# Performance work log

Hardware: AMD Instinct MI355X
Metric: run time of the kernel (lower is better)

Reference implementation:

```python
import jax, jax.numpy as jnp
import numpy as np

B, N, K, IN = 8, 2048, 8, 5
BN = B * N

def _lin(k, i, o):
    s = 1.0 / np.sqrt(i)
    return jax.random.uniform(k, (i, o), jnp.float32, -s, s)

def setup_inputs() -> dict:
    key = jax.random.key(0)
    ks = jax.random.split(key, 12)
    inp = {"points": jax.random.normal(ks[0], (B, N, IN), jnp.float32)}
    dims = [(IN * 2, 64), (64 * 2, 128), (128 * 2, 256)]
    for n, (i, o) in enumerate(dims, 1):
        inp[f"W{n}"] = _lin(ks[n], i, o)
        inp[f"b{n}"] = jnp.zeros((o,), jnp.float32)
        inp[f"g{n}"] = jnp.ones((o,), jnp.float32)
        inp[f"be{n}"] = jnp.zeros((o,), jnp.float32)
    inp["Wf1"] = _lin(ks[10], 448, 512); inp["bf1"] = jnp.zeros((512,), jnp.float32)
    inp["gf"] = jnp.ones((512,), jnp.float32); inp["bef"] = jnp.zeros((512,), jnp.float32)
    inp["Wf2"] = _lin(ks[11], 512, 128); inp["bf2"] = jnp.zeros((128,), jnp.float32)
    return inp

def _lrelu(x):
    return jnp.where(x >= 0, x, 0.2 * x)

def _bn(x, g, b, eps=1e-5):
    # BatchNorm1d in training mode: per-feature batch statistics
    m = x.mean(0)
    v = x.var(0)
    return (x - m) * jax.lax.rsqrt(v + eps) * g + b

def _knn_idx(pos):
    # pos: [B,N,3] -> neighbor indices [B,N,K], self excluded
    sq = (pos * pos).sum(-1)
    d = sq[:, :, None] + sq[:, None, :] - 2.0 * jnp.einsum('bnc,bmc->bnm', pos, pos)
    d = d + jnp.eye(N, dtype=d.dtype) * 1e10  # exclude self
    _, idx = jax.lax.top_k(-d, K)
    return idx

def _edge_conv(x, src, dst, W, b, g, be):
    # PyG EdgeConv: msg = nn(cat[x_i, x_j - x_i]); aggr='max' at target i
    xc = x[dst]
    xn = x[src]
    h = jnp.concatenate([xc, xn - xc], axis=-1) @ W + b
    h = _bn(_lrelu(h), g, be)
    return jax.ops.segment_max(h, dst, num_segments=BN)

def reference(points, W1, b1, g1, be1, W2, b2, g2, be2, W3, b3, g3, be3,
              Wf1, bf1, gf, bef, Wf2, bf2):
    pos = points[..., :3]                      # [B,N,3]
    idx = _knn_idx(pos)                        # [B,N,K]
    offs = (jnp.arange(B) * N)[:, None, None]
    src = (idx + offs).reshape(-1)             # neighbor (source) node ids [E]
    dst = jnp.repeat(jnp.arange(BN), K)        # center (target) node ids [E]
    x = points.reshape(BN, IN)
    x1 = _edge_conv(x, src, dst, W1, b1, g1, be1)   # [BN,64]
    x2 = _edge_conv(x1, src, dst, W2, b2, g2, be2)  # [BN,128]
    x3 = _edge_conv(x2, src, dst, W3, b3, g3, be3)  # [BN,256]
    xs = jnp.concatenate([x1, x2, x3], axis=-1).reshape(B, N, 448)
    gfeat = xs.max(axis=1)                     # global max pool per cloud [B,448]
    h = _bn(_lrelu(gfeat @ Wf1 + bf1), gf, bef)
    return h @ Wf2 + bf2                       # [B,128]
```

## Files before the change

kernel.cpp:

```cpp
#include <hip/hip_runtime.h>
#include <math.h>

#define B_ 8
#define N_ 2048
#define K_ 8
#define IN_ 5
#define BN_ (B_*N_)
#define NEDGE_ (BN_*K_)
#define GRP 8
#define SEG_ 32
#define CSEG_ (N_/SEG_)
#define CHUNKS_ (N_/GRP)

typedef unsigned short ushort8_ __attribute__((ext_vector_type(8)));
typedef short bf16x8_ __attribute__((ext_vector_type(8)));
typedef float f32x4_ __attribute__((ext_vector_type(4)));

__device__ inline unsigned short f2bf(float f) {
    unsigned int u = __float_as_uint(f);
    u += 0x7fffu + ((u >> 16) & 1u);
    return (unsigned short)(u >> 16);
}
__device__ inline float bf2f(unsigned short h) {
    return __uint_as_float(((unsigned int)h) << 16);
}

__device__ inline unsigned int ord_f32(float f) {
    unsigned int u = __float_as_uint(f);
    return u ^ (((unsigned int)((int)u >> 31)) | 0x80000000u);
}

__global__ __launch_bounds__(256) void knn_part(const float4* __restrict__ P4,
                                                unsigned long long* __restrict__ part) {
    int tid = threadIdx.x;
    int bblk = blockIdx.x >> 3;
    int q = blockIdx.x * 256 + tid;
    int nloc = q & (N_-1);
    int seg = blockIdx.y;

    float4 qp = P4[q];
    float qx2 = -2.0f*qp.x, qy2 = -2.0f*qp.y, qz2 = -2.0f*qp.z;
    float qsq = qp.w;

    unsigned int bd[K_], bi[K_];
#pragma unroll
    for (int k = 0; k < K_; ++k) { bd[k] = 0xFFFFFFFFu; bi[k] = 0xFFFFFFFFu; }

    const float4* __restrict__ cb = P4 + ((size_t)bblk << 11) + (size_t)seg*CSEG_;
    int jbase = seg * CSEG_;

#pragma unroll 8
    for (int jj = 0; jj < CSEG_; ++jj) {
        float4 c = cb[jj];
        float d = qsq + c.w;
        d = fmaf(qx2, c.x, d);
        d = fmaf(qy2, c.y, d);
        d = fmaf(qz2, c.z, d);
        int jg = jbase + jj;
        d = (jg == nloc) ? INFINITY : d;
        unsigned int cd = ord_f32(d);
        unsigned int ci = (unsigned int)jg;
#pragma unroll
        for (int p = 0; p < K_; ++p) {
            bool lt = cd < bd[p];
            unsigned int nd = lt ? cd : bd[p];
            unsigned int xd = lt ? bd[p] : cd;
            unsigned int ni = lt ? ci : bi[p];
            unsigned int xi = lt ? bi[p] : ci;
            bd[p] = nd; cd = xd; bi[p] = ni; ci = xi;
        }
    }
    unsigned long long* op = part + ((size_t)seg * BN_ + q) * K_;
#pragma unroll
    for (int k = 0; k < K_; ++k)
        op[k] = ((unsigned long long)bd[k] << 32) | bi[k];
}

__global__ __launch_bounds__(128) void knn_merge(const unsigned long long* __restrict__ part,
                                                 int* __restrict__ src) {
    int q = blockIdx.x * 128 + threadIdx.x;
    int b = q / N_;
    unsigned long long best[K_];
#pragma unroll
    for (int k = 0; k < K_; ++k) best[k] = ~0ull;
    for (int s = 0; s < SEG_; ++s) {
        const unsigned long long* lp = part + ((size_t)s * BN_ + q) * K_;
#pragma unroll
        for (int k = 0; k < K_; ++k) {
            unsigned long long key = lp[k];
            if (key >= best[K_-1]) break;
            unsigned long long cur = key;
#pragma unroll
            for (int p = 0; p < K_; ++p) {
                unsigned long long lo = best[p] < cur ? best[p] : cur;
                unsigned long long hi = best[p] < cur ? cur : best[p];
                best[p] = lo; cur = hi;
            }
        }
    }
#pragma unroll
    for (int k = 0; k < K_; ++k)
        src[(size_t)q*K_ + k] = b*N_ + (int)(best[k] & 0xFFFFFFFFu);
}

__global__ __launch_bounds__(256) void cast_prep1(const float* __restrict__ X,
                                                  unsigned short* __restrict__ Xh,
                                                  unsigned short* __restrict__ Xl,
                                                  float4* __restrict__ P4,
                                                  const float* __restrict__ W1,
                                                  const float* __restrict__ b1,
                                                  unsigned short* __restrict__ WTh,
                                                  unsigned short* __restrict__ WTl,
                                                  float* __restrict__ cvec) {
    const int total8 = BN_ * 32 / 8;
    int t = blockIdx.x * 256 + threadIdx.x;
    if (t < total8) {
        int m = t >> 2;
        int k0 = (t & 3) * 8;
        ushort8_ vh, vl;
#pragma unroll
        for (int j = 0; j < 8; ++j) {
            int k = k0 + j;
            float v = (k < IN_) ? X[(size_t)m*IN_ + k] : 0.0f;
            unsigned short h = f2bf(v);
            vh[j] = h;
            vl[j] = f2bf(v - bf2f(h));
        }
        *(ushort8_*)(Xh + (size_t)m*32 + k0) = vh;
        *(ushort8_*)(Xl + (size_t)m*32 + k0) = vl;
        if (t < BN_) {
            const float* p = X + (size_t)t*IN_;
            float x = p[0], y = p[1], z = p[2];
            P4[t] = make_float4(x, y, z, x*x + y*y + z*z);
        }
    } else {
        int idx = t - total8;
        const int nWT = 2*64*32;
        if (idx < nWT) {
            int n = idx >> 5;
            int k = idx & 31;
            float val = 0.0f;
            if (k < IN_) {
                if (n < 64) val = W1[(size_t)k*64 + n] - W1[(size_t)(IN_+k)*64 + n];
                else        val = W1[(size_t)(IN_+k)*64 + (n - 64)];
            }
            unsigned short h = f2bf(val);
            WTh[(size_t)n*32 + k] = h;
            WTl[(size_t)n*32 + k] = f2bf(val - bf2f(h));
        } else if (idx < nWT + 64) {
            int c = idx - nWT;
            cvec[c] = b1[c];
        }
    }
}

__global__ __launch_bounds__(256) void prep_layer(const float* __restrict__ W,
                                                  const float* __restrict__ scale,
                                                  const float* __restrict__ shift,
                                                  const float* __restrict__ bias,
                                                  unsigned short* __restrict__ WTh,
                                                  unsigned short* __restrict__ WTl,
                                                  float* __restrict__ cvec,
                                                  int Cin, int C, int Kpad) {
    int idx = blockIdx.x * 256 + threadIdx.x;
    int nWT = 2*C*Kpad;
    if (idx < nWT) {
        int n = idx / Kpad;
        int k = idx % Kpad;
        float val = 0.0f;
        if (k < Cin) {
            float s = scale[k];
            if (n < C) val = s * (W[(size_t)k*C + n] - W[(size_t)(Cin+k)*C + n]);
            else       val = s * W[(size_t)(Cin+k)*C + (n - C)];
        }
        unsigned short h = f2bf(val);
        WTh[(size_t)n*Kpad + k] = h;
        WTl[(size_t)n*Kpad + k] = f2bf(val - bf2f(h));
    } else if (idx < nWT + C) {
        int c = idx - nWT;
        float acc = bias[c];
        for (int d = 0; d < Cin; ++d) acc += shift[d] * W[(size_t)d*C + c];
        cvec[c] = acc;
    }
}

__global__ __launch_bounds__(256) void mfma_dual(const unsigned short* __restrict__ Xh,
                                                 const unsigned short* __restrict__ Xl,
                                                 const unsigned short* __restrict__ WTh,
                                                 const unsigned short* __restrict__ WTl,
                                                 float* __restrict__ PQ, int K, int Ntot,
                                                 int gx) {
    __shared__ unsigned short sXh[128*32], sXl[128*32], sWh[128*32], sWl[128*32];
    int n = blockIdx.x;
    int by = (n & 7) + 8*(n/(8*gx));
    int bx = (n >> 3) % gx;
    int tid = threadIdx.x, l = tid & 63, w = tid >> 6;
    int wr = w >> 1, wc = w & 1;
    int bm = by * 128, bn0 = bx * 128;

    f32x4_ acc[4][4];
#pragma unroll
    for (int i = 0; i < 4; ++i)
#pragma unroll
        for (int j = 0; j < 4; ++j) acc[i][j] = (f32x4_){0.f, 0.f, 0.f, 0.f};

    for (int k0 = 0; k0 < K; k0 += 32) {
#pragma unroll
        for (int i = 0; i < 2; ++i) {
            int idx = tid + i*256;
            int row = idx >> 2;
            int col0 = (idx & 3) * 8;
            size_t gxo = (size_t)(bm  + row)*K + k0 + col0;
            size_t gwo = (size_t)(bn0 + row)*K + k0 + col0;
            int lo_ = ((row << 6) | (col0 << 1)) ^ ((row & 7) << 4);
            *(ushort8_*)((char*)sXh + lo_) = *(const ushort8_*)(Xh + gxo);
            *(ushort8_*)((char*)sXl + lo_) = *(const ushort8_*)(Xl + gxo);
            *(ushort8_*)((char*)sWh + lo_) = *(const ushort8_*)(WTh + gwo);
            *(ushort8_*)((char*)sWl + lo_) = *(const ushort8_*)(WTl + gwo);
        }
        __syncthreads();

        int kb = (l >> 4) << 4;
        bf16x8_ bh[4], bl4[4];
#pragma unroll
        for (int nf = 0; nf < 4; ++nf) {
            int rn = wc*64 + nf*16 + (l & 15);
            int o = ((rn << 6) | kb) ^ ((rn & 7) << 4);
            bh[nf]  = *(const bf16x8_*)((const char*)sWh + o);
            bl4[nf] = *(const bf16x8_*)((const char*)sWl + o);
        }
#pragma unroll
        for (int mf = 0; mf < 4; ++mf) {
            int rm = wr*64 + mf*16 + (l & 15);
            int o = ((rm << 6) | kb) ^ ((rm & 7) << 4);
            bf16x8_ ah = *(const bf16x8_*)((const char*)sXh + o);
            bf16x8_ al = *(const bf16x8_*)((const char*)sXl + o);
#pragma unroll
            for (int nf = 0; nf < 4; ++nf) {
                acc[mf][nf] = __builtin_amdgcn_mfma_f32_16x16x32_bf16(ah, bh[nf],  acc[mf][nf], 0, 0, 0);
                acc[mf][nf] = __builtin_amdgcn_mfma_f32_16x16x32_bf16(ah, bl4[nf], acc[mf][nf], 0, 0, 0);
                acc[mf][nf] = __builtin_amdgcn_mfma_f32_16x16x32_bf16(al, bh[nf],  acc[mf][nf], 0, 0, 0);
            }
        }
        __syncthreads();
    }

    int r0 = (l >> 4) << 2, cB = l & 15;
#pragma unroll
    for (int mf = 0; mf < 4; ++mf)
#pragma unroll
        for (int nf = 0; nf < 4; ++nf) {
            int col = bn0 + wc*64 + nf*16 + cB;
#pragma unroll
            for (int reg = 0; reg < 4; ++reg) {
                int row = bm + wr*64 + mf*16 + r0 + reg;
                PQ[(size_t)row*Ntot + col] = acc[mf][nf][reg];
            }
        }
}

__global__ void combine_kernel(const float* __restrict__ P, const float* __restrict__ Q,
                               const float* __restrict__ cvec, const int* __restrict__ src,
                               unsigned short* __restrict__ Xh_out, unsigned short* __restrict__ Xl_out,
                               float* __restrict__ partial, float* __restrict__ gpart,
                               int C, int S) {
    int pb = blockIdx.x;
    int lb = (pb & 7) * CHUNKS_ + (pb >> 3);
    int c = threadIdx.x;
    int i0 = lb * GRP;
    float cv = cvec[c];
    float sum = 0.f, ssq = 0.f;
    float bmx = -INFINITY;
    for (int g = 0; g < GRP; ++g) {
        int i = i0 + g;
        float p = P[(size_t)i*S + c] + cv;
        float mx = -INFINITY;
#pragma unroll
        for (int k = 0; k < K_; ++k) {
            int s = src[(size_t)i*K_ + k];
            float h = p + Q[(size_t)s*S + c];
            float l = (h >= 0.f) ? h : 0.2f*h;
            sum += l; ssq += l*l;
            mx = fmaxf(mx, l);
        }
        if (Xh_out) {
            unsigned short hh = f2bf(mx);
            Xh_out[(size_t)i*C + c] = hh;
            Xl_out[(size_t)i*C + c] = f2bf(mx - bf2f(hh));
        }
        bmx = fmaxf(bmx, mx);
    }
    gpart[(size_t)lb*C + c] = bmx;
    partial[(size_t)lb*2*C + c]     = sum;
    partial[(size_t)lb*2*C + C + c] = ssq;
}

__global__ __launch_bounds__(256) void reduce_kernel(const float* __restrict__ partial, int nblocks, int C,
                              const float* __restrict__ g, const float* __restrict__ be,
                              float* __restrict__ scale, float* __restrict__ shift) {
    int c = blockIdx.x;
    float s0 = 0.f, s1 = 0.f;
    for (int blk = threadIdx.x; blk < nblocks; blk += 256) {
        s0 += partial[(size_t)blk*2*C + c];
        s1 += partial[(size_t)blk*2*C + C + c];
    }
    __shared__ float l0[256], l1[256];
    l0[threadIdx.x] = s0; l1[threadIdx.x] = s1;
    __syncthreads();
    for (int off = 128; off > 0; off >>= 1) {
        if (threadIdx.x < off) {
            l0[threadIdx.x] += l0[threadIdx.x + off];
            l1[threadIdx.x] += l1[threadIdx.x + off];
        }
        __syncthreads();
    }
    if (threadIdx.x == 0) {
        float mean = l0[0] / (float)NEDGE_;
        float var  = l1[0] / (float)NEDGE_ - mean*mean;
        float sc = g[c] * rsqrtf(var + 1e-5f);
        scale[c] = sc;
        shift[c] = be[c] - mean*sc;
    }
}

__global__ __launch_bounds__(1024) void gmax_finalize(
        const float* __restrict__ gp1, const float* __restrict__ gp2, const float* __restrict__ gp3,
        const float* __restrict__ sc1, const float* __restrict__ sh1,
        const float* __restrict__ sc2, const float* __restrict__ sh2,
        const float* __restrict__ sc3, const float* __restrict__ sh3,
        float* __restrict__ gfeat) {
    int b = blockIdx.x, grp = blockIdx.y;
    const float *gp, *sc, *sh; int C, c0, coff;
    if (grp == 0)      { gp = gp1; sc = sc1; sh = sh1; C = 64;  c0 = 0;            coff = 0;   }
    else if (grp <= 2) { gp = gp2; sc = sc2; sh = sh2; C = 128; c0 = (grp-1)*64;   coff = 64;  }
    else               { gp = gp3; sc = sc3; sh = sh3; C = 256; c0 = (grp-3)*64;   coff = 192; }
    int cl = threadIdx.x & 63;
    int stripe = threadIdx.x >> 6;
    int c = c0 + cl;
    float mx = -INFINITY;
    for (int ch = stripe; ch < CHUNKS_; ch += 16)
        mx = fmaxf(mx, gp[((size_t)b*CHUNKS_ + ch)*C + c]);
    __shared__ float red[16][64];
    red[stripe][cl] = mx;
    __syncthreads();
    for (int off = 8; off > 0; off >>= 1) {
        if (stripe < off) red[stripe][cl] = fmaxf(red[stripe][cl], red[stripe+off][cl]);
        __syncthreads();
    }
    if (stripe == 0)
        gfeat[b*448 + coff + c] = sc[c]*red[0][cl] + sh[c];
}

__global__ __launch_bounds__(256) void final1(const float* __restrict__ gfeat,
                                              const float* __restrict__ Wf1, const float* __restrict__ bf1,
                                              const float* __restrict__ gf, const float* __restrict__ bef,
                                              float* __restrict__ H) {
    __shared__ float gfs[B_][448];
    __shared__ float red[4][64][B_];
    int t = threadIdx.x;
    int cl = t & 63;
    int stripe = t >> 6;
    int c = blockIdx.x * 64 + cl;
    for (int e = t; e < B_*448; e += 256) gfs[e/448][e%448] = gfeat[e];
    __syncthreads();
    float acc[B_] = {};
    for (int d = stripe*112; d < stripe*112 + 112; ++d) {
        float w = Wf1[(size_t)d*512 + c];
#pragma unroll
        for (int r = 0; r < B_; ++r) acc[r] += gfs[r][d] * w;
    }
#pragma unroll
    for (int r = 0; r < B_; ++r) red[stripe][cl][r] = acc[r];
    __syncthreads();
    if (stripe == 0) {
        float v[B_];
        float b1v = bf1[c];
#pragma unroll
        for (int r = 0; r < B_; ++r) {
            float a = red[0][cl][r] + red[1][cl][r] + red[2][cl][r] + red[3][cl][r] + b1v;
            v[r] = (a >= 0.f) ? a : 0.2f*a;
        }
        float mean = 0.f;
#pragma unroll
        for (int r = 0; r < B_; ++r) mean += v[r];
        mean *= (1.0f/B_);
        float var = 0.f;
#pragma unroll
        for (int r = 0; r < B_; ++r) { float dd = v[r] - mean; var += dd*dd; }
        var *= (1.0f/B_);
        float sc = gf[c] * rsqrtf(var + 1e-5f);
        float sh = bef[c] - mean*sc;
#pragma unroll
        for (int r = 0; r < B_; ++r) H[(size_t)r*512 + c] = v[r]*sc + sh;
    }
}

__global__ __launch_bounds__(128) void final2(const float* __restrict__ H,
                                              const float* __restrict__ Wf2, const float* __restrict__ bf2,
                                              float* __restrict__ out) {
    int b = blockIdx.x, c = threadIdx.x;
    __shared__ float hs[512];
    for (int e = c; e < 512; e += 128) hs[e] = H[(size_t)b*512 + e];
    __syncthreads();
    float a = bf2[c];
    for (int d = 0; d < 512; ++d) a += hs[d] * Wf2[(size_t)d*128 + c];
    out[b*128 + c] = a;
}

extern "C" void kernel_launch(void* const* d_in, const int* in_sizes, int n_in,
                              void* d_out, int out_size, void* d_ws, size_t ws_size,
                              hipStream_t stream) {
    (void)in_sizes; (void)n_in; (void)out_size; (void)ws_size;
    const float* points = (const float*)d_in[0];
    const float* W1 = (const float*)d_in[1];  const float* b1 = (const float*)d_in[2];
    const float* g1 = (const float*)d_in[3];  const float* be1 = (const float*)d_in[4];
    const float* W2 = (const float*)d_in[5];  const float* b2 = (const float*)d_in[6];
    const float* g2 = (const float*)d_in[7];  const float* be2 = (const float*)d_in[8];
    const float* W3 = (const float*)d_in[9];  const float* b3 = (const float*)d_in[10];
    const float* g3 = (const float*)d_in[11]; const float* be3 = (const float*)d_in[12];
    const float* Wf1 = (const float*)d_in[13]; const float* bf1 = (const float*)d_in[14];
    const float* gf = (const float*)d_in[15];  const float* bef = (const float*)d_in[16];
    const float* Wf2 = (const float*)d_in[17]; const float* bf2 = (const float*)d_in[18];
    float* out = (float*)d_out;

    size_t off = 0;
    char* base = (char*)d_ws;
    auto carve = [&](size_t bytes) -> void* {
        void* p = base + off;
        off += (bytes + 255) & ~(size_t)255;
        return p;
    };
    int*   src     = (int*)  carve((size_t)NEDGE_ * 4);
    float* PQ      = (float*)carve((size_t)BN_ * 512 * 4);
    float* gp1     = (float*)carve((size_t)(BN_/GRP) * 64 * 4);
    float* gp2     = (float*)carve((size_t)(BN_/GRP) * 128 * 4);
    float* gp3     = (float*)carve((size_t)(BN_/GRP) * 256 * 4);
    unsigned short* XhA = (unsigned short*)carve((size_t)BN_ * 128 * 2);
    unsigned short* XlA = (unsigned short*)carve((size_t)BN_ * 128 * 2);
    unsigned short* XhB = (unsigned short*)carve((size_t)BN_ * 128 * 2);
    unsigned short* XlB = (unsigned short*)carve((size_t)BN_ * 128 * 2);
    unsigned short* WTh = (unsigned short*)carve((size_t)512 * 128 * 2);
    unsigned short* WTl = (unsigned short*)carve((size_t)512 * 128 * 2);
    float4* P4     = (float4*)carve((size_t)BN_ * 16);
    float* cvec    = (float*)carve(256 * 4);
    float* sc1     = (float*)carve(64 * 4);
    float* sh1     = (float*)carve(64 * 4);
    float* sc2     = (float*)carve(128 * 4);
    float* sh2     = (float*)carve(128 * 4);
    float* sc3     = (float*)carve(256 * 4);
    float* sh3     = (float*)carve(256 * 4);
    float* partial = (float*)carve((size_t)(BN_/GRP) * 2 * 256 * 4);
    float* gfeat   = (float*)carve((size_t)B_ * 448 * 4);
    float* H       = (float*)carve((size_t)B_ * 512 * 4);

    cast_prep1<<<(65536 + 4096 + 64 + 255)/256, 256, 0, stream>>>(
        points, XhA, XlA, P4, W1, b1, WTh, WTl, cvec);

    unsigned long long* part = (unsigned long long*)PQ;
    knn_part<<<dim3(BN_/256, SEG_), 256, 0, stream>>>(P4, part);
    knn_merge<<<BN_/128, 128, 0, stream>>>(part, src);

    mfma_dual<<<1*(BN_/128), 256, 0, stream>>>(XhA, XlA, WTh, WTl, PQ, 32, 128, 1);
    combine_kernel<<<BN_/GRP, 64, 0, stream>>>(PQ, PQ + 64, cvec, src, XhB, XlB, partial, gp1, 64, 128);
    reduce_kernel<<<64, 256, 0, stream>>>(partial, BN_/GRP, 64, g1, be1, sc1, sh1);

    prep_layer<<<(2*128*64 + 128 + 255)/256, 256, 0, stream>>>(W2, sc1, sh1, b2, WTh, WTl, cvec, 64, 128, 64);
    mfma_dual<<<2*(BN_/128), 256, 0, stream>>>(XhB, XlB, WTh, WTl, PQ, 64, 256, 2);
    combine_kernel<<<BN_/GRP, 128, 0, stream>>>(PQ, PQ + 128, cvec, src, XhA, XlA, partial, gp2, 128, 256);
    reduce_kernel<<<128, 256, 0, stream>>>(partial, BN_/GRP, 128, g2, be2, sc2, sh2);

    prep_layer<<<(2*256*128 + 256 + 255)/256, 256, 0, stream>>>(W3, sc2, sh2, b3, WTh, WTl, cvec, 128, 256, 128);
    mfma_dual<<<4*(BN_/128), 256, 0, stream>>>(XhA, XlA, WTh, WTl, PQ, 128, 512, 4);
    combine_kernel<<<BN_/GRP, 256, 0, stream>>>(PQ, PQ + 256, cvec, src, nullptr, nullptr, partial, gp3, 256, 512);
    reduce_kernel<<<256, 256, 0, stream>>>(partial, BN_/GRP, 256, g3, be3, sc3, sh3);

    gmax_finalize<<<dim3(B_, 7), 1024, 0, stream>>>(gp1, gp2, gp3,
                                                    sc1, sh1, sc2, sh2, sc3, sh3, gfeat);

    final1<<<8, 256, 0, stream>>>(gfeat, Wf1, bf1, gf, bef, H);
    final2<<<8, 128, 0, stream>>>(H, Wf2, bf2, out);
}
```

Measured before the change: 220.4 us.

## Fuse BN stats reduction with weight prep and widen combine blocks

The per-channel BN reduction and the next layer's weight folding are merged into one bnprep kernel, cutting two launches. The bias/shift constant vector is now computed inside combine_kernel, so the separate cvec pass goes away. combine_kernel always runs 256 threads and splits the points of a group across sub-groups, then does an in-block shared-memory reduction. This raises occupancy for the narrow layers, but every block now redundantly recomputes the cvec dot product. The kNN distance key also drops the order-preserving float transform and compares raw bits, which assumes distances are non-negative.

```diff
diff --git a/kernel.cpp b/kernel.cpp
--- a/kernel.cpp
+++ b/kernel.cpp
@@ -25,11 +25,6 @@
     return __uint_as_float(((unsigned int)h) << 16);
 }
 
-__device__ inline unsigned int ord_f32(float f) {
-    unsigned int u = __float_as_uint(f);
-    return u ^ (((unsigned int)((int)u >> 31)) | 0x80000000u);
-}
-
 __global__ __launch_bounds__(256) void knn_part(const float4* __restrict__ P4,
                                                 unsigned long long* __restrict__ part) {
     int tid = threadIdx.x;
@@ -56,9 +51,9 @@
         d = fmaf(qx2, c.x, d);
         d = fmaf(qy2, c.y, d);
         d = fmaf(qz2, c.z, d);
+        unsigned int cd = __float_as_uint(d);
         int jg = jbase + jj;
-        d = (jg == nloc) ? INFINITY : d;
-        unsigned int cd = ord_f32(d);
+        cd = (jg == nloc) ? 0xFFFFFFFFu : cd;
         unsigned int ci = (unsigned int)jg;
 #pragma unroll
         for (int p = 0; p < K_; ++p) {
@@ -108,10 +103,8 @@
                                                   unsigned short* __restrict__ Xl,
                                                   float4* __restrict__ P4,
                                                   const float* __restrict__ W1,
-                                                  const float* __restrict__ b1,
                                                   unsigned short* __restrict__ WTh,
-                                                  unsigned short* __restrict__ WTl,
-                                                  float* __restrict__ cvec) {
+                                                  unsigned short* __restrict__ WTl) {
     const int total8 = BN_ * 32 / 8;
     int t = blockIdx.x * 256 + threadIdx.x;
     if (t < total8) {
@@ -147,40 +140,76 @@
             unsigned short h = f2bf(val);
             WTh[(size_t)n*32 + k] = h;
             WTl[(size_t)n*32 + k] = f2bf(val - bf2f(h));
-        } else if (idx < nWT + 64) {
-            int c = idx - nWT;
-            cvec[c] = b1[c];
-        }
-    }
-}
-
-__global__ __launch_bounds__(256) void prep_layer(const float* __restrict__ W,
-                                                  const float* __restrict__ scale,
-                                                  const float* __restrict__ shift,
-                                                  const float* __restrict__ bias,
-                                                  unsigned short* __restrict__ WTh,
-                                                  unsigned short* __restrict__ WTl,
-                                                  float* __restrict__ cvec,
-                                                  int Cin, int C, int Kpad) {
-    int idx = blockIdx.x * 256 + threadIdx.x;
-    int nWT = 2*C*Kpad;
-    if (idx < nWT) {
-        int n = idx / Kpad;
-        int k = idx % Kpad;
-        float val = 0.0f;
-        if (k < Cin) {
-            float s = scale[k];
-            if (n < C) val = s * (W[(size_t)k*C + n] - W[(size_t)(Cin+k)*C + n]);
-            else       val = s * W[(size_t)(Cin+k)*C + (n - C)];
-        }
+        }
+    }
+}
+
+__global__ __launch_bounds__(256) void bnprep(const float* __restrict__ partial, int nblocks, int Cprev,
+                                              const float* __restrict__ g, const float* __restrict__ be,
+                                              float* __restrict__ scale, float* __restrict__ shift,
+                                              const float* __restrict__ W, int C, int Kpad,
+                                              unsigned short* __restrict__ WTh,
+                                              unsigned short* __restrict__ WTl) {
+    int k = blockIdx.x;
+    int t = threadIdx.x;
+    float s0 = 0.f, s1 = 0.f;
+    for (int blk = t; blk < nblocks; blk += 256) {
+        s0 += partial[(size_t)blk*2*Cprev + k];
+        s1 += partial[(size_t)blk*2*Cprev + Cprev + k];
+    }
+    __shared__ float l0[256], l1[256];
+    __shared__ float sc_s;
+    l0[t] = s0; l1[t] = s1;
+    __syncthreads();
+    for (int off = 128; off > 0; off >>= 1) {
+        if (t < off) { l0[t] += l0[t + off]; l1[t] += l1[t + off]; }
+        __syncthreads();
+    }
+    if (t == 0) {
+        float mean = l0[0] / (float)NEDGE_;
+        float var  = l1[0] / (float)NEDGE_ - mean*mean;
+        float sc = g[k] * rsqrtf(var + 1e-5f);
+        scale[k] = sc;
+        shift[k] = be[k] - mean*sc;
+        sc_s = sc;
+    }
+    __syncthreads();
+    float s = sc_s;
+    for (int n = t; n < 2*C; n += 256) {
+        float val;
+        if (n < C) val = s * (W[(size_t)k*C + n] - W[(size_t)(Cprev+k)*C + n]);
+        else       val = s * W[(size_t)(Cprev+k)*C + (n - C)];
         unsigned short h = f2bf(val);
         WTh[(size_t)n*Kpad + k] = h;
         WTl[(size_t)n*Kpad + k] = f2bf(val - bf2f(h));
-    } else if (idx < nWT + C) {
-        int c = idx - nWT;
-        float acc = bias[c];
-        for (int d = 0; d < Cin; ++d) acc += shift[d] * W[(size_t)d*C + c];
-        cvec[c] = acc;
+    }
+}
+
+__global__ __launch_bounds__(256) void reduce_kernel(const float* __restrict__ partial, int nblocks, int C,
+                              const float* __restrict__ g, const float* __restrict__ be,
+                              float* __restrict__ scale, float* __restrict__ shift) {
+    int c = blockIdx.x;
+    float s0 = 0.f, s1 = 0.f;
+    for (int blk = threadIdx.x; blk < nblocks; blk += 256) {
+        s0 += partial[(size_t)blk*2*C + c];
+        s1 += partial[(size_t)blk*2*C + C + c];
+    }
+    __shared__ float l0[256], l1[256];
+    l0[threadIdx.x] = s0; l1[threadIdx.x] = s1;
+    __syncthreads();
+    for (int off = 128; off > 0; off >>= 1) {
+        if (threadIdx.x < off) {
+            l0[threadIdx.x] += l0[threadIdx.x + off];
+            l1[threadIdx.x] += l1[threadIdx.x + off];
+        }
+        __syncthreads();
+    }
+    if (threadIdx.x == 0) {
+        float mean = l0[0] / (float)NEDGE_;
+        float var  = l1[0] / (float)NEDGE_ - mean*mean;
+        float sc = g[c] * rsqrtf(var + 1e-5f);
+        scale[c] = sc;
+        shift[c] = be[c] - mean*sc;
     }
 }
 
@@ -259,20 +288,29 @@
         }
 }
 
-__global__ void combine_kernel(const float* __restrict__ P, const float* __restrict__ Q,
-                               const float* __restrict__ cvec, const int* __restrict__ src,
-                               unsigned short* __restrict__ Xh_out, unsigned short* __restrict__ Xl_out,
-                               float* __restrict__ partial, float* __restrict__ gpart,
-                               int C, int S) {
+__global__ __launch_bounds__(256) void combine_kernel(
+        const float* __restrict__ P, const float* __restrict__ Q,
+        const int* __restrict__ src,
+        unsigned short* __restrict__ Xh_out, unsigned short* __restrict__ Xl_out,
+        float* __restrict__ partial, float* __restrict__ gpart,
+        const float* __restrict__ W, const float* __restrict__ bias,
+        const float* __restrict__ shift, int Cin,
+        int C, int S) {
     int pb = blockIdx.x;
     int lb = (pb & 7) * CHUNKS_ + (pb >> 3);
-    int c = threadIdx.x;
-    int i0 = lb * GRP;
-    float cv = cvec[c];
+    int tid = threadIdx.x;
+    int c = tid & (C - 1);
+    int g = tid / C;
+    int PPG = GRP / (256 / C);
+    float cv = bias[c];
+    if (shift)
+        for (int d = 0; d < Cin; ++d) cv += shift[d] * W[(size_t)d*C + c];
+
+    int i0 = lb * GRP + g * PPG;
     float sum = 0.f, ssq = 0.f;
     float bmx = -INFINITY;
-    for (int g = 0; g < GRP; ++g) {
-        int i = i0 + g;
+    for (int gg = 0; gg < PPG; ++gg) {
+        int i = i0 + gg;
         float p = P[(size_t)i*S + c] + cv;
         float mx = -INFINITY;
 #pragma unroll
@@ -290,36 +328,21 @@
         }
         bmx = fmaxf(bmx, mx);
     }
-    gpart[(size_t)lb*C + c] = bmx;
-    partial[(size_t)lb*2*C + c]     = sum;
-    partial[(size_t)lb*2*C + C + c] = ssq;
-}
-
-__global__ __launch_bounds__(256) void reduce_kernel(const float* __restrict__ partial, int nblocks, int C,
-                              const float* __restrict__ g, const float* __restrict__ be,
-                              float* __restrict__ scale, float* __restrict__ shift) {
-    int c = blockIdx.x;
-    float s0 = 0.f, s1 = 0.f;
-    for (int blk = threadIdx.x; blk < nblocks; blk += 256) {
-        s0 += partial[(size_t)blk*2*C + c];
-        s1 += partial[(size_t)blk*2*C + C + c];
-    }
-    __shared__ float l0[256], l1[256];
-    l0[threadIdx.x] = s0; l1[threadIdx.x] = s1;
-    __syncthreads();
-    for (int off = 128; off > 0; off >>= 1) {
-        if (threadIdx.x < off) {
-            l0[threadIdx.x] += l0[threadIdx.x + off];
-            l1[threadIdx.x] += l1[threadIdx.x + off];
+    __shared__ float s0[256], s1[256], s2[256];
+    s0[tid] = sum; s1[tid] = ssq; s2[tid] = bmx;
+    __syncthreads();
+    for (int off = 128; off >= C; off >>= 1) {
+        if (tid < off) {
+            s0[tid] += s0[tid + off];
+            s1[tid] += s1[tid + off];
+            s2[tid] = fmaxf(s2[tid], s2[tid + off]);
         }
         __syncthreads();
     }
-    if (threadIdx.x == 0) {
-        float mean = l0[0] / (float)NEDGE_;
-        float var  = l1[0] / (float)NEDGE_ - mean*mean;
-        float sc = g[c] * rsqrtf(var + 1e-5f);
-        scale[c] = sc;
-        shift[c] = be[c] - mean*sc;
+    if (tid < C) {
+        gpart[(size_t)lb*C + c] = s2[tid];
+        partial[(size_t)lb*2*C + c]     = s0[tid];
+        partial[(size_t)lb*2*C + C + c] = s1[tid];
     }
 }
 
@@ -442,7 +465,6 @@
     unsigned short* WTh = (unsigned short*)carve((size_t)512 * 128 * 2);
     unsigned short* WTl = (unsigned short*)carve((size_t)512 * 128 * 2);
     float4* P4     = (float4*)carve((size_t)BN_ * 16);
-    float* cvec    = (float*)carve(256 * 4);
     float* sc1     = (float*)carve(64 * 4);
     float* sh1     = (float*)carve(64 * 4);
     float* sc2     = (float*)carve(128 * 4);
@@ -453,25 +475,26 @@
     float* gfeat   = (float*)carve((size_t)B_ * 448 * 4);
     float* H       = (float*)carve((size_t)B_ * 512 * 4);
 
-    cast_prep1<<<(65536 + 4096 + 64 + 255)/256, 256, 0, stream>>>(
-        points, XhA, XlA, P4, W1, b1, WTh, WTl, cvec);
+    cast_prep1<<<(65536 + 4096 + 255)/256, 256, 0, stream>>>(
+        points, XhA, XlA, P4, W1, WTh, WTl);
 
     unsigned long long* part = (unsigned long long*)PQ;
     knn_part<<<dim3(BN_/256, SEG_), 256, 0, stream>>>(P4, part);
     knn_merge<<<BN_/128, 128, 0, stream>>>(part, src);
 
     mfma_dual<<<1*(BN_/128), 256, 0, stream>>>(XhA, XlA, WTh, WTl, PQ, 32, 128, 1);
-    combine_kernel<<<BN_/GRP, 64, 0, stream>>>(PQ, PQ + 64, cvec, src, XhB, XlB, partial, gp1, 64, 128);
-    reduce_kernel<<<64, 256, 0, stream>>>(partial, BN_/GRP, 64, g1, be1, sc1, sh1);
-
-    prep_layer<<<(2*128*64 + 128 + 255)/256, 256, 0, stream>>>(W2, sc1, sh1, b2, WTh, WTl, cvec, 64, 128, 64);
+    combine_kernel<<<BN_/GRP, 256, 0, stream>>>(PQ, PQ + 64, src, XhB, XlB, partial, gp1,
+                                                W1, b1, nullptr, IN_, 64, 128);
+    bnprep<<<64, 256, 0, stream>>>(partial, BN_/GRP, 64, g1, be1, sc1, sh1,
+                                   W2, 128, 64, WTh, WTl);
     mfma_dual<<<2*(BN_/128), 256, 0, stream>>>(XhB, XlB, WTh, WTl, PQ, 64, 256, 2);
-    combine_kernel<<<BN_/GRP, 128, 0, stream>>>(PQ, PQ + 128, cvec, src, XhA, XlA, partial, gp2, 128, 256);
-    reduce_kernel<<<128, 256, 0, stream>>>(partial, BN_/GRP, 128, g2, be2, sc2, sh2);
-
-    prep_layer<<<(2*256*128 + 256 + 255)/256, 256, 0, stream>>>(W3, sc2, sh2, b3, WTh, WTl, cvec, 128, 256, 128);
+    combine_kernel<<<BN_/GRP, 256, 0, stream>>>(PQ, PQ + 128, src, XhA, XlA, partial, gp2,
+                                                W2, b2, sh1, 64, 128, 256);
+    bnprep<<<128, 256, 0, stream>>>(partial, BN_/GRP, 128, g2, be2, sc2, sh2,
+                                    W3, 256, 128, WTh, WTl);
     mfma_dual<<<4*(BN_/128), 256, 0, stream>>>(XhA, XlA, WTh, WTl, PQ, 128, 512, 4);
-    combine_kernel<<<BN_/GRP, 256, 0, stream>>>(PQ, PQ + 256, cvec, src, nullptr, nullptr, partial, gp3, 256, 512);
+    combine_kernel<<<BN_/GRP, 256, 0, stream>>>(PQ, PQ + 256, src, nullptr, nullptr, partial, gp3,
+                                                W3, b3, sh2, 128, 256, 512);
     reduce_kernel<<<256, 256, 0, stream>>>(partial, BN_/GRP, 256, g3, be3, sc3, sh3);
 
     gmax_finalize<<<dim3(B_, 7), 1024, 0, stream>>>(gp1, gp2, gp3,
```

New measurement: 246.7 us. 11.9% more time.
